# Performance work log

Hardware: AMD Instinct MI355X
Metric: run time of the kernel (lower is better)

## Reference

```python
import jax, jax.numpy as jnp
import numpy as np

H = 8  # heads, hard-coded in the original module


def setup_inputs() -> dict:
    key = jax.random.key(0)
    ks = jax.random.split(key, 7)
    B, Lq, Lkv = 4, 2048, 512
    dim_q, dim_kv = 1024, 768
    q = jax.random.normal(ks[0], (B, Lq, dim_q), dtype=jnp.float32)
    kv = jax.random.normal(ks[1], (B, Lkv, dim_kv), dtype=jnp.float32)
    # Linear weights stored as [in, out] so y = x @ W (math-equivalent to torch Linear)
    Wq = jax.random.normal(ks[2], (dim_q, dim_q), dtype=jnp.float32) / np.sqrt(dim_q)
    Wk = jax.random.normal(ks[3], (dim_kv, dim_q), dtype=jnp.float32) / np.sqrt(dim_kv)
    Wv = jax.random.normal(ks[4], (dim_kv, dim_q), dtype=jnp.float32) / np.sqrt(dim_kv)
    Wo = jax.random.normal(ks[5], (dim_q, dim_q), dtype=jnp.float32) / np.sqrt(dim_q)
    bo = jax.random.normal(ks[6], (dim_q,), dtype=jnp.float32) * 0.01
    return {"q": q, "kv": kv, "Wq": Wq, "Wk": Wk, "Wv": Wv, "Wo": Wo, "bo": bo}


def reference(q, kv, Wq, Wk, Wv, Wo, bo):
    B, Lq, dim_q = q.shape
    hd = dim_q // H
    scale = jnp.asarray(hd, q.dtype) ** -0.5
    # projections
    qp = q @ Wq   # [B, Lq, dim_q]
    kp = kv @ Wk  # [B, Lkv, dim_q]
    vp = kv @ Wv  # [B, Lkv, dim_q]
    # split heads: [B, L, H, hd]
    qh = qp.reshape(B, Lq, H, hd)
    kh = kp.reshape(B, kv.shape[1], H, hd)
    vh = vp.reshape(B, kv.shape[1], H, hd)
    # scaled attention scores and softmax
    scores = jnp.einsum("bqhd,bkhd->bhqk", qh, kh) * scale
    attn = jax.nn.softmax(scores, axis=-1)
    out = jnp.einsum("bhqk,bkhd->bqhd", attn, vh).reshape(B, Lq, dim_q)
    return out @ Wo + bo
```

## Files before the change

kernel.cpp:

```cpp
#include <hip/hip_runtime.h>
#include <hip/hip_cooperative_groups.h>

namespace cg = cooperative_groups;


typedef unsigned short u16;
typedef unsigned int u32;
using short8  = __attribute__((ext_vector_type(8))) short;
using floatx4 = __attribute__((ext_vector_type(4))) float;

__device__ inline u16 f2bf(float x) {
  union { float f; u32 u; } v; v.f = x;
  u32 r = (v.u + 0x7fffu + ((v.u >> 16) & 1u)) >> 16;
  return (u16)r;
}

__device__ inline float fast_exp2(float x) {
#if __has_builtin(__builtin_amdgcn_exp2f)
  return __builtin_amdgcn_exp2f(x);
#else
  return exp2f(x);
#endif
}

#define MFMA(a, b, c) __builtin_amdgcn_mfma_f32_16x16x32_bf16(a, b, c, 0, 0, 0)

__device__ inline void async_lds16(const void* g, void* l) {
  __builtin_amdgcn_global_load_lds(
      (const __attribute__((address_space(1))) void*)g,
      (__attribute__((address_space(3))) void*)l, 16, 0, 0);
}

__global__ void cvt_all(const float* __restrict__ q, const float* __restrict__ kv,
                        u16* __restrict__ q_bf, u16* __restrict__ kv_bf) {
  int i = blockIdx.x * 256 + threadIdx.x;
  const float* src; u16* dst; int idx;
  if (i < 1048576) { src = q;  dst = q_bf;  idx = i; }
  else             { src = kv; dst = kv_bf; idx = i - 1048576; }
  float4 a = ((const float4*)src)[2 * idx];
  float4 b = ((const float4*)src)[2 * idx + 1];
  u16 t[8] = {f2bf(a.x), f2bf(a.y), f2bf(a.z), f2bf(a.w),
              f2bf(b.x), f2bf(b.y), f2bf(b.z), f2bf(b.w)};
  ((short8*)dst)[idx] = *(short8*)t;
}

__global__ __launch_bounds__(256)
void transpose_all(const float* __restrict__ Wq, const float* __restrict__ Wk,
                   const float* __restrict__ Wv, const float* __restrict__ Wo,
                   u16* __restrict__ WqT, u16* __restrict__ WkvT, u16* __restrict__ WoT) {
  __shared__ float tile[64][68];
  const int z = blockIdx.z;
  const float* W; u16* Wt; int K;
  if      (z == 0) { W = Wq; Wt = WqT;               K = 1024; }
  else if (z == 1) { W = Wk; Wt = WkvT;              K = 768;  }
  else if (z == 2) { W = Wv; Wt = WkvT + 1024 * 768; K = 768;  }
  else             { W = Wo; Wt = WoT;               K = 1024; }
  const int k0 = blockIdx.y * 64, n0 = blockIdx.x * 64;
  if (k0 >= K) return;
  const int N = 1024;
  const int t = threadIdx.x;
  for (int p = 0; p < 4; ++p) {
    int cid = p * 256 + t;
    int row = cid >> 4, c = cid & 15;
    float4 v = *(const float4*)&W[(long)(k0 + row) * N + n0 + c * 4];
    tile[row][c * 4 + 0] = v.x; tile[row][c * 4 + 1] = v.y;
    tile[row][c * 4 + 2] = v.z; tile[row][c * 4 + 3] = v.w;
  }
  __syncthreads();
  for (int p = 0; p < 2; ++p) {
    int oc = p * 256 + t;
    int n = oc >> 3, c = oc & 7;
    u16 tmp[8];
    for (int s = 0; s < 8; ++s) tmp[s] = f2bf(tile[c * 8 + s][n]);
    *(short8*)&Wt[(long)(n0 + n) * K + k0 + c * 8] = *(short8*)tmp;
  }
}

__device__ __forceinline__
void gemm_body(const u16* __restrict__ A, const u16* __restrict__ Bt,
               u16* __restrict__ Cb, float* __restrict__ Cf,
               const float* __restrict__ bias, u16* __restrict__ vt_out,
               int K, int ldc, int lin, int mt_per_xcd, u16* smem) {
  u16* As = smem;
  u16* Bs = smem + 8192;
  const int tid  = threadIdx.x;
  const int wave = tid >> 6, lane = tid & 63;
  const int l15  = lane & 15, quad = lane >> 4;
  const int wm   = (wave >> 1) * 64, wn = (wave & 1) * 64;
  const int xcd  = lin & 7, slot = lin >> 3;
  const int mt   = xcd * mt_per_xcd + (slot % mt_per_xcd);
  const int nti  = slot / mt_per_xcd;
  const long m0  = (long)mt * 128, n0 = (long)nti * 128;
  const int lrow = lane >> 3;
  const int lk   = (lane & 7) * 8;

  floatx4 acc[4][4] = {};

  for (int k0 = 0; k0 < K; k0 += 64) {
    for (int c = 0; c < 4; ++c) {
      int rbase = (wave * 4 + c) * 8;
      async_lds16(A  + (m0 + rbase + lrow) * (long)K + k0 + lk, &As[(wave * 4 + c) * 512]);
      async_lds16(Bt + (n0 + rbase + lrow) * (long)K + k0 + lk, &Bs[(wave * 4 + c) * 512]);
    }
    __syncthreads();
    for (int kc = 0; kc < 2; ++kc) {
      short8 af[4], bfr[4];
      for (int i = 0; i < 4; ++i)
        af[i] = *(const short8*)&As[(wm + i * 16 + l15) * 64 + kc * 32 + quad * 8];
      for (int j = 0; j < 4; ++j)
        bfr[j] = *(const short8*)&Bs[(wn + j * 16 + l15) * 64 + kc * 32 + quad * 8];
      for (int i = 0; i < 4; ++i)
        for (int j = 0; j < 4; ++j)
          acc[i][j] = MFMA(af[i], bfr[j], acc[i][j]);
    }
    __syncthreads();
  }

  if (Cf) {
    for (int i = 0; i < 4; ++i)
      for (int j = 0; j < 4; ++j) {
        long row = m0 + wm + i * 16 + quad * 4;
        long col = n0 + wn + j * 16 + l15;
        float b = bias ? bias[col] : 0.f;
        for (int r = 0; r < 4; ++r) Cf[(row + r) * (long)ldc + col] = acc[i][j][r] + b;
      }
    return;
  }
  for (int i = 0; i < 4; ++i)
    for (int j = 0; j < 4; ++j)
      for (int r = 0; r < 4; ++r)
        smem[(wm + i * 16 + quad * 4 + r) * 138 + wn + j * 16 + l15] = f2bf(acc[i][j][r]);
  __syncthreads();
  if (vt_out && nti >= 8) {
    const int h  = nti - 8;
    const int bq = (int)(m0 >> 9);
    const int l0 = (int)(m0 & 511);
    u16* vbase = vt_out + ((long)(bq * 8 + h) * 128) * 512;
    for (int p = 0; p < 8; ++p) {
      int cid = p * 256 + tid;
      int d = cid >> 4, c = cid & 15;
      u16 tmp[8];
      for (int s = 0; s < 8; ++s) tmp[s] = smem[(c * 8 + s) * 138 + d];
      *(short8*)&vbase[(long)d * 512 + l0 + c * 8] = *(short8*)tmp;
    }
  } else {
    for (int p = 0; p < 8; ++p) {
      int cid = p * 256 + tid;
      int row = cid >> 4, c = cid & 15;
      short8 v = *(const short8*)&smem[row * 138 + c * 8];
      *(short8*)&Cb[(m0 + row) * (long)ldc + n0 + c * 8] = v;
    }
  }
}

__device__ __forceinline__
void attn_body(const u16* __restrict__ qp, const u16* __restrict__ kp,
               const u16* __restrict__ vT, u16* __restrict__ ctx,
               int lin, u16* smem) {
  u16* Ks = smem;
  u16* Vs = smem + 8192;
  const int tid  = threadIdx.x;
  const int wave = tid >> 6, lane = tid & 63;
  u16* Pw = smem + 16384 + wave * 1024;
  const int l15  = lane & 15, quad = lane >> 4;
  const int xcd  = lin & 7, slot = lin >> 3;
  const int pairIdx = xcd * 4 + (slot & 3);
  const int b = pairIdx >> 3, h = pairIdx & 7;
  const int qtile = slot >> 2;
  const long rowbase = (long)b * 2048 + qtile * 64 + wave * 16;
  const float sc = 0.08838834764831845f * 1.4426950408889634f;

  short8 aQ[4];
  for (int dc = 0; dc < 4; ++dc)
    aQ[dc] = *(const short8*)&qp[(rowbase + l15) * 1024 + h * 128 + dc * 32 + quad * 8];

  floatx4 O[8] = {};
  float lsum[4] = {};
  const u16* kpb   = kp + ((long)b * 512) * 1024 + h * 128;
  const u16* vbase = vT + ((long)(b * 8 + h) * 128) * 512;

  const int krow = lane >> 4;
  const int kpos = lane & 15;
  const int vrow = lane >> 3;
  const int vpos = lane & 7;

  for (int t = 0; t < 8; ++t) {
    for (int i = 0; i < 4; ++i) {
      int inst = wave * 4 + i;
      int row  = inst * 4 + krow;
      int g    = kpos ^ (row & 15);
      async_lds16(kpb + (long)(t * 64 + row) * 1024 + g * 8, &Ks[inst * 512]);
    }
    for (int i = 0; i < 4; ++i) {
      int inst = wave * 4 + i;
      int d    = inst * 8 + vrow;
      int g    = vpos ^ (d & 7);
      async_lds16(vbase + (long)d * 512 + t * 64 + g * 8, &Vs[inst * 512]);
    }
    __syncthreads();

    floatx4 S[4] = {};
    for (int dc = 0; dc < 4; ++dc)
      for (int ks = 0; ks < 4; ++ks) {
        int k = ks * 16 + l15;
        short8 bk = *(const short8*)&Ks[k * 128 + (((dc * 4 + quad) ^ l15) * 8)];
        S[ks] = MFMA(aQ[dc], bk, S[ks]);
      }
    for (int ks = 0; ks < 4; ++ks)
      for (int r = 0; r < 4; ++r) {
        float p = fast_exp2(S[ks][r] * sc);
        lsum[r] += p;
        int row = quad * 4 + r;
        int g   = (ks * 2 + (l15 >> 3)) ^ (row & 7);
        Pw[row * 64 + g * 8 + (l15 & 7)] = f2bf(p);
      }
    short8 aP[2];
    for (int kc = 0; kc < 2; ++kc)
      aP[kc] = *(const short8*)&Pw[l15 * 64 + (((kc * 4 + quad) ^ (l15 & 7)) * 8)];
    for (int j = 0; j < 8; ++j) {
      int d = j * 16 + l15;
      short8 bV0 = *(const short8*)&Vs[d * 64 + ((quad ^ (l15 & 7)) * 8)];
      short8 bV1 = *(const short8*)&Vs[d * 64 + (((4 + quad) ^ (l15 & 7)) * 8)];
      O[j] = MFMA(aP[0], bV0, O[j]);
      O[j] = MFMA(aP[1], bV1, O[j]);
    }
    __syncthreads();
  }

  for (int r = 0; r < 4; ++r) {
    float sum = lsum[r];
    for (int off = 1; off < 16; off <<= 1) sum += __shfl_xor(sum, off);
    lsum[r] = 1.f / sum;
  }
  for (int j = 0; j < 8; ++j)
    for (int r = 0; r < 4; ++r)
      ctx[(rowbase + quad * 4 + r) * 1024 + h * 128 + j * 16 + l15] =
          f2bf(O[j][r] * lsum[r]);
}

__global__ __launch_bounds__(256, 4)
void mega(const u16* q_bf, const u16* WqT, const u16* kv_bf, const u16* WkvT,
          const u16* WoT, u16* qp, u16* kp, u16* vT, u16* ctx,
          float* out, const float* bo) {
  __shared__ u16 smem[20480];
  cg::grid_group g = cg::this_grid();
  const int bid = blockIdx.x;

  if (bid < 768) {
    const bool isQ = bid < 512;
    gemm_body(isQ ? q_bf : kv_bf, isQ ? WqT : WkvT, isQ ? qp : kp,
              nullptr, nullptr, isQ ? (u16*)nullptr : vT,
              isQ ? 1024 : 768, 1024, isQ ? bid : bid - 512, isQ ? 8 : 2, smem);
  }
  g.sync();
  attn_body(qp, kp, vT, ctx, bid, smem);
  g.sync();
  if (bid < 512)
    gemm_body(ctx, WoT, nullptr, out, bo, nullptr, 1024, 1024, bid, 8, smem);
}

__global__ __launch_bounds__(256)
void k_proj_q(const u16* __restrict__ q_bf, const u16* __restrict__ WqT,
              u16* __restrict__ qp) {
  __shared__ u16 smem[17664];
  gemm_body(q_bf, WqT, qp, nullptr, nullptr, nullptr, 1024, 1024, blockIdx.x, 8, smem);
}
__global__ __launch_bounds__(256)
void k_proj_kv(const u16* __restrict__ kv_bf, const u16* __restrict__ WkvT,
               u16* __restrict__ kp, u16* __restrict__ vT) {
  __shared__ u16 smem[17664];
  gemm_body(kv_bf, WkvT, kp, nullptr, nullptr, vT, 768, 1024, blockIdx.x, 2, smem);
}
__global__ __launch_bounds__(256, 4)
void k_attn(const u16* __restrict__ qp, const u16* __restrict__ kp,
            const u16* __restrict__ vT, u16* __restrict__ ctx) {
  __shared__ u16 smem[20480];
  attn_body(qp, kp, vT, ctx, blockIdx.x, smem);
}
__global__ __launch_bounds__(256)
void k_oproj(const u16* __restrict__ ctx, const u16* __restrict__ WoT,
             float* __restrict__ out, const float* __restrict__ bo) {
  __shared__ u16 smem[17664];
  gemm_body(ctx, WoT, nullptr, out, bo, nullptr, 1024, 1024, blockIdx.x, 8, smem);
}

extern "C" void kernel_launch(void* const* d_in, const int* in_sizes, int n_in,
                              void* d_out, int out_size, void* d_ws, size_t ws_size,
                              hipStream_t stream) {
  const float* q  = (const float*)d_in[0];
  const float* kv = (const float*)d_in[1];
  const float* Wq = (const float*)d_in[2];
  const float* Wk = (const float*)d_in[3];
  const float* Wv = (const float*)d_in[4];
  const float* Wo = (const float*)d_in[5];
  const float* bo = (const float*)d_in[6];
  float* out = (float*)d_out;

  char* ws = (char*)d_ws;
  u16* q_bf  = (u16*)(ws + 0);
  u16* kv_bf = (u16*)(ws + 16777216);
  u16* WqT   = (u16*)(ws + 19922944);
  u16* WkvT  = (u16*)(ws + 22020096);
  u16* WoT   = (u16*)(ws + 25165824);
  u16* qp    = (u16*)(ws + 27262976);
  u16* kp    = (u16*)(ws + 44040192);
  u16* vT    = (u16*)(ws + 52428800);
  u16* ctx   = (u16*)(ws + 56623104);

  cvt_all<<<4864, 256, 0, stream>>>(q, kv, q_bf, kv_bf);
  transpose_all<<<dim3(16, 16, 4), 256, 0, stream>>>(Wq, Wk, Wv, Wo, WqT, WkvT, WoT);

  int maxb = 0;
  hipError_t oe = hipOccupancyMaxActiveBlocksPerMultiprocessor(
      &maxb, (const void*)mega, 256, 0);
  if (oe == hipSuccess && maxb >= 4) {
    void* args[] = {(void*)&q_bf, (void*)&WqT, (void*)&kv_bf, (void*)&WkvT,
                    (void*)&WoT, (void*)&qp, (void*)&kp, (void*)&vT,
                    (void*)&ctx, (void*)&out, (void*)&bo};
    hipLaunchCooperativeKernel((const void*)mega, dim3(1024), dim3(256),
                               args, 0, stream);
  } else {
    k_proj_q<<<512, 256, 0, stream>>>(q_bf, WqT, qp);
    k_proj_kv<<<256, 256, 0, stream>>>(kv_bf, WkvT, kp, vT);
    k_attn<<<1024, 256, 0, stream>>>(qp, kp, vT, ctx);
    k_oproj<<<512, 256, 0, stream>>>(ctx, WoT, out, bo);
  }
}
```

Measured before the change: 211.6 us.

## Fold conversion and weight transpose into cooperative kernel; XOR-swizzle GEMM LDS tiles

Moves the fp32→bf16 input conversion and the weight transpose-conversion into the cooperative mega kernel as a first phase followed by a grid sync. This removes two separate kernel launches and the gaps between them. The GEMM LDS layout now uses an XOR swizzle on the 16-byte k-chunks, applied to both the async global→LDS writes and the fragment reads, to reduce bank conflicts. The cost is one extra grid-wide barrier and transpose work that shares smem with the later phases.

```diff
diff --git a/kernel.cpp b/kernel.cpp
--- a/kernel.cpp
+++ b/kernel.cpp
@@ -31,31 +31,33 @@
       (__attribute__((address_space(3))) void*)l, 16, 0, 0);
 }
 
-__global__ void cvt_all(const float* __restrict__ q, const float* __restrict__ kv,
-                        u16* __restrict__ q_bf, u16* __restrict__ kv_bf) {
-  int i = blockIdx.x * 256 + threadIdx.x;
-  const float* src; u16* dst; int idx;
-  if (i < 1048576) { src = q;  dst = q_bf;  idx = i; }
-  else             { src = kv; dst = kv_bf; idx = i - 1048576; }
-  float4 a = ((const float4*)src)[2 * idx];
-  float4 b = ((const float4*)src)[2 * idx + 1];
-  u16 t[8] = {f2bf(a.x), f2bf(a.y), f2bf(a.z), f2bf(a.w),
-              f2bf(b.x), f2bf(b.y), f2bf(b.z), f2bf(b.w)};
-  ((short8*)dst)[idx] = *(short8*)t;
-}
-
-__global__ __launch_bounds__(256)
-void transpose_all(const float* __restrict__ Wq, const float* __restrict__ Wk,
-                   const float* __restrict__ Wv, const float* __restrict__ Wo,
-                   u16* __restrict__ WqT, u16* __restrict__ WkvT, u16* __restrict__ WoT) {
-  __shared__ float tile[64][68];
-  const int z = blockIdx.z;
+__device__ __forceinline__
+void cvt_body(const float* __restrict__ q, const float* __restrict__ kv,
+              u16* __restrict__ q_bf, u16* __restrict__ kv_bf, int lin) {
+  for (int i = lin * 256 + (int)threadIdx.x; i < 1245184; i += 262144) {
+    const float* src; u16* dst; int idx;
+    if (i < 1048576) { src = q;  dst = q_bf;  idx = i; }
+    else             { src = kv; dst = kv_bf; idx = i - 1048576; }
+    float4 a = ((const float4*)src)[2 * idx];
+    float4 b = ((const float4*)src)[2 * idx + 1];
+    u16 t[8] = {f2bf(a.x), f2bf(a.y), f2bf(a.z), f2bf(a.w),
+                f2bf(b.x), f2bf(b.y), f2bf(b.z), f2bf(b.w)};
+    ((short8*)dst)[idx] = *(short8*)t;
+  }
+}
+
+__device__ __forceinline__
+void transpose_body(int bid, const float* __restrict__ Wq, const float* __restrict__ Wk,
+                    const float* __restrict__ Wv, const float* __restrict__ Wo,
+                    u16* __restrict__ WqT, u16* __restrict__ WkvT, u16* __restrict__ WoT,
+                    float* __restrict__ tile ) {
+  const int z = bid >> 8;
   const float* W; u16* Wt; int K;
   if      (z == 0) { W = Wq; Wt = WqT;               K = 1024; }
   else if (z == 1) { W = Wk; Wt = WkvT;              K = 768;  }
   else if (z == 2) { W = Wv; Wt = WkvT + 1024 * 768; K = 768;  }
   else             { W = Wo; Wt = WoT;               K = 1024; }
-  const int k0 = blockIdx.y * 64, n0 = blockIdx.x * 64;
+  const int k0 = ((bid >> 4) & 15) * 64, n0 = (bid & 15) * 64;
   if (k0 >= K) return;
   const int N = 1024;
   const int t = threadIdx.x;
@@ -63,15 +65,15 @@
     int cid = p * 256 + t;
     int row = cid >> 4, c = cid & 15;
     float4 v = *(const float4*)&W[(long)(k0 + row) * N + n0 + c * 4];
-    tile[row][c * 4 + 0] = v.x; tile[row][c * 4 + 1] = v.y;
-    tile[row][c * 4 + 2] = v.z; tile[row][c * 4 + 3] = v.w;
+    tile[row * 68 + c * 4 + 0] = v.x; tile[row * 68 + c * 4 + 1] = v.y;
+    tile[row * 68 + c * 4 + 2] = v.z; tile[row * 68 + c * 4 + 3] = v.w;
   }
   __syncthreads();
   for (int p = 0; p < 2; ++p) {
     int oc = p * 256 + t;
     int n = oc >> 3, c = oc & 7;
     u16 tmp[8];
-    for (int s = 0; s < 8; ++s) tmp[s] = f2bf(tile[c * 8 + s][n]);
+    for (int s = 0; s < 8; ++s) tmp[s] = f2bf(tile[(c * 8 + s) * 68 + n]);
     *(short8*)&Wt[(long)(n0 + n) * K + k0 + c * 8] = *(short8*)tmp;
   }
 }
@@ -92,7 +94,8 @@
   const int nti  = slot / mt_per_xcd;
   const long m0  = (long)mt * 128, n0 = (long)nti * 128;
   const int lrow = lane >> 3;
-  const int lk   = (lane & 7) * 8;
+  const int lk   = (((lane & 7) ^ lrow) * 8);
+  const int r7   = l15 & 7;
 
   floatx4 acc[4][4] = {};
 
@@ -106,9 +109,9 @@
     for (int kc = 0; kc < 2; ++kc) {
       short8 af[4], bfr[4];
       for (int i = 0; i < 4; ++i)
-        af[i] = *(const short8*)&As[(wm + i * 16 + l15) * 64 + kc * 32 + quad * 8];
+        af[i] = *(const short8*)&As[(wm + i * 16 + l15) * 64 + (((kc * 4 + quad) ^ r7) * 8)];
       for (int j = 0; j < 4; ++j)
-        bfr[j] = *(const short8*)&Bs[(wn + j * 16 + l15) * 64 + kc * 32 + quad * 8];
+        bfr[j] = *(const short8*)&Bs[(wn + j * 16 + l15) * 64 + (((kc * 4 + quad) ^ r7) * 8)];
       for (int i = 0; i < 4; ++i)
         for (int j = 0; j < 4; ++j)
           acc[i][j] = MFMA(af[i], bfr[j], acc[i][j]);
@@ -239,12 +242,17 @@
 }
 
 __global__ __launch_bounds__(256, 4)
-void mega(const u16* q_bf, const u16* WqT, const u16* kv_bf, const u16* WkvT,
-          const u16* WoT, u16* qp, u16* kp, u16* vT, u16* ctx,
-          float* out, const float* bo) {
-  __shared__ u16 smem[20480];
+void mega(const float* q, const float* kv, const float* Wq, const float* Wk,
+          const float* Wv, const float* Wo,
+          u16* q_bf, u16* kv_bf, u16* WqT, u16* WkvT, u16* WoT,
+          u16* qp, u16* kp, u16* vT, u16* ctx, float* out, const float* bo) {
+  __shared__ __align__(16) u16 smem[20480];
   cg::grid_group g = cg::this_grid();
   const int bid = blockIdx.x;
+
+  cvt_body(q, kv, q_bf, kv_bf, bid);
+  transpose_body(bid, Wq, Wk, Wv, Wo, WqT, WkvT, WoT, (float*)smem);
+  g.sync();
 
   if (bid < 768) {
     const bool isQ = bid < 512;
@@ -259,28 +267,48 @@
     gemm_body(ctx, WoT, nullptr, out, bo, nullptr, 1024, 1024, bid, 8, smem);
 }
 
+__global__ void cvt_all(const float* __restrict__ q, const float* __restrict__ kv,
+                        u16* __restrict__ q_bf, u16* __restrict__ kv_bf) {
+  int i = blockIdx.x * 256 + threadIdx.x;
+  const float* src; u16* dst; int idx;
+  if (i < 1048576) { src = q;  dst = q_bf;  idx = i; }
+  else             { src = kv; dst = kv_bf; idx = i - 1048576; }
+  float4 a = ((const float4*)src)[2 * idx];
+  float4 b = ((const float4*)src)[2 * idx + 1];
+  u16 t[8] = {f2bf(a.x), f2bf(a.y), f2bf(a.z), f2bf(a.w),
+              f2bf(b.x), f2bf(b.y), f2bf(b.z), f2bf(b.w)};
+  ((short8*)dst)[idx] = *(short8*)t;
+}
+__global__ __launch_bounds__(256)
+void transpose_all(const float* __restrict__ Wq, const float* __restrict__ Wk,
+                   const float* __restrict__ Wv, const float* __restrict__ Wo,
+                   u16* __restrict__ WqT, u16* __restrict__ WkvT, u16* __restrict__ WoT) {
+  __shared__ __align__(16) float tile[64 * 68];
+  int bid = blockIdx.x + blockIdx.y * 16 + blockIdx.z * 256;
+  transpose_body(bid, Wq, Wk, Wv, Wo, WqT, WkvT, WoT, tile);
+}
 __global__ __launch_bounds__(256)
 void k_proj_q(const u16* __restrict__ q_bf, const u16* __restrict__ WqT,
               u16* __restrict__ qp) {
-  __shared__ u16 smem[17664];
+  __shared__ __align__(16) u16 smem[17664];
   gemm_body(q_bf, WqT, qp, nullptr, nullptr, nullptr, 1024, 1024, blockIdx.x, 8, smem);
 }
 __global__ __launch_bounds__(256)
 void k_proj_kv(const u16* __restrict__ kv_bf, const u16* __restrict__ WkvT,
                u16* __restrict__ kp, u16* __restrict__ vT) {
-  __shared__ u16 smem[17664];
+  __shared__ __align__(16) u16 smem[17664];
   gemm_body(kv_bf, WkvT, kp, nullptr, nullptr, vT, 768, 1024, blockIdx.x, 2, smem);
 }
 __global__ __launch_bounds__(256, 4)
 void k_attn(const u16* __restrict__ qp, const u16* __restrict__ kp,
             const u16* __restrict__ vT, u16* __restrict__ ctx) {
-  __shared__ u16 smem[20480];
+  __shared__ __align__(16) u16 smem[20480];
   attn_body(qp, kp, vT, ctx, blockIdx.x, smem);
 }
 __global__ __launch_bounds__(256)
 void k_oproj(const u16* __restrict__ ctx, const u16* __restrict__ WoT,
              float* __restrict__ out, const float* __restrict__ bo) {
-  __shared__ u16 smem[17664];
+  __shared__ __align__(16) u16 smem[17664];
   gemm_body(ctx, WoT, nullptr, out, bo, nullptr, 1024, 1024, blockIdx.x, 8, smem);
 }
 
@@ -307,19 +335,20 @@
   u16* vT    = (u16*)(ws + 52428800);
   u16* ctx   = (u16*)(ws + 56623104);
 
-  cvt_all<<<4864, 256, 0, stream>>>(q, kv, q_bf, kv_bf);
-  transpose_all<<<dim3(16, 16, 4), 256, 0, stream>>>(Wq, Wk, Wv, Wo, WqT, WkvT, WoT);
-
   int maxb = 0;
   hipError_t oe = hipOccupancyMaxActiveBlocksPerMultiprocessor(
       &maxb, (const void*)mega, 256, 0);
   if (oe == hipSuccess && maxb >= 4) {
-    void* args[] = {(void*)&q_bf, (void*)&WqT, (void*)&kv_bf, (void*)&WkvT,
-                    (void*)&WoT, (void*)&qp, (void*)&kp, (void*)&vT,
-                    (void*)&ctx, (void*)&out, (void*)&bo};
+    void* args[] = {(void*)&q,    (void*)&kv,    (void*)&Wq,   (void*)&Wk,
+                    (void*)&Wv,   (void*)&Wo,    (void*)&q_bf, (void*)&kv_bf,
+                    (void*)&WqT,  (void*)&WkvT,  (void*)&WoT,  (void*)&qp,
+                    (void*)&kp,   (void*)&vT,    (void*)&ctx,  (void*)&out,
+                    (void*)&bo};
     hipLaunchCooperativeKernel((const void*)mega, dim3(1024), dim3(256),
                                args, 0, stream);
   } else {
+    cvt_all<<<4864, 256, 0, stream>>>(q, kv, q_bf, kv_bf);
+    transpose_all<<<dim3(16, 16, 4), 256, 0, stream>>>(Wq, Wk, Wv, Wo, WqT, WkvT, WoT);
     k_proj_q<<<512, 256, 0, stream>>>(q_bf, WqT, qp);
     k_proj_kv<<<256, 256, 0, stream>>>(kv_bf, WkvT, kp, vT);
     k_attn<<<1024, 256, 0, stream>>>(qp, kp, vT, ctx);
```

Result: faster. 200.6 us (-5.2%).
